# Optimization experiments

Hardware: AMD Instinct MI355X
Metric: run time of the kernel (lower is better)

Reference implementation:

```python
import jax, jax.numpy as jnp
import numpy as np
import math

B, L, D, P = 2, 2048, 256, 32
PI = math.pi


def _layernorm(x, g, b, eps=1e-5):
    m = x.mean(-1, keepdims=True)
    v = x.var(-1, keepdims=True)
    return (x - m) / jnp.sqrt(v + eps) * g + b


def setup_inputs() -> dict:
    key = jax.random.key(0)
    ks = jax.random.split(key, 16)
    sd = 1.0 / math.sqrt(D)
    f32 = jnp.float32
    inp = {
        "x": jax.random.normal(ks[0], (B, L, D), f32),
        # key_encoder: Linear(D, P)
        "key_W": jax.random.normal(ks[1], (D, P), f32) * sd,
        "key_b": jnp.zeros((P,), f32),
        # value_encoder: Linear(D, D)
        "val_W": jax.random.normal(ks[2], (D, D), f32) * sd,
        "val_b": jnp.zeros((D,), f32),
        # refiner: LayerNorm(D), Linear(D, 2D), GELU, Linear(2D, D)
        "ln1_g": jnp.ones((D,), f32),
        "ln1_b": jnp.zeros((D,), f32),
        "W1": jax.random.normal(ks[3], (D, 2 * D), f32) * sd,
        "b1": jnp.zeros((2 * D,), f32),
        "W2": jax.random.normal(ks[4], (2 * D, D), f32) * (1.0 / math.sqrt(2 * D)),
        "b2": jnp.zeros((D,), f32),
        # to_out: LayerNorm(D), Linear(D, D)
        "ln2_g": jnp.ones((D,), f32),
        "ln2_b": jnp.zeros((D,), f32),
        "Wo": jax.random.normal(ks[5], (D, D), f32) * sd,
        "bo": jnp.zeros((D,), f32),
    }
    return inp


def reference(x, key_W, key_b, val_W, val_b, ln1_g, ln1_b, W1, b1, W2, b2,
              ln2_g, ln2_b, Wo, bo):
    # key phases in (-pi, pi); phasor exp(i*theta) handled as (cos, sin)
    phases = jnp.tanh(x @ key_W + key_b) * PI          # (B, L, P)
    values = x @ val_W + val_b                          # (B, L, D)

    cos_p = jnp.cos(phases)
    sin_p = jnp.sin(phases)
    # torch.roll(shifts=1, dims=1) then zero the first position -> shift right, row 0 = 0
    zrow = jnp.zeros_like(cos_p[:, :1])
    cos_s = jnp.concatenate([zrow, cos_p[:, :-1]], axis=1)
    sin_s = jnp.concatenate([zrow, sin_p[:, :-1]], axis=1)

    # odd positions hold values
    vmask = (jnp.arange(L) % 2 == 1).astype(x.dtype)    # (L,)
    mv = values * vmask[None, :, None]                  # (B, L, D)

    # bind: outer product phasor (P) x value (D); real/imag parts
    bound_re = cos_s[..., None] * mv[:, :, None, :]     # (B, L, P, D)
    bound_im = sin_s[..., None] * mv[:, :, None, :]
    mem_re = jnp.cumsum(bound_re, axis=1)
    mem_im = jnp.cumsum(bound_im, axis=1)

    # retrieve: Re[ memory * exp(-i*theta) ] summed over phases
    retrieved = (jnp.einsum('blpd,blp->bld', mem_re, cos_p)
                 + jnp.einsum('blpd,blp->bld', mem_im, sin_p))

    valid = jnp.maximum(jnp.cumsum(vmask), 1.0)         # (L,)
    retrieved = retrieved / (jnp.sqrt(valid)[None, :, None] * math.sqrt(P))

    h = _layernorm(retrieved, ln1_g, ln1_b)
    h = jax.nn.gelu(h @ W1 + b1, approximate=False)
    refined = h @ W2 + b2
    out = x + (_layernorm(refined, ln2_g, ln2_b) @ Wo + bo)
    return out
```

## Files before the change

### kernel.cpp

```cpp
#include <hip/hip_runtime.h>
#include <math.h>

#define BB 2
#define LL 2048
#define DD 256
#define PP 32
#define NC 64
#define PI_F 3.14159265358979323846f

typedef __attribute__((ext_vector_type(8))) short bf16x8;
typedef __attribute__((ext_vector_type(4))) float f32x4;
typedef unsigned short ushort_t;
typedef unsigned int uint_t;

__device__ inline ushort_t f2bf(float x) {
    uint_t u = __float_as_uint(x);
    uint_t r = (u + 0x7fffu + ((u >> 16) & 1u)) >> 16;
    return (ushort_t)r;
}

__global__ __launch_bounds__(256) void prep_key_kernel(
    const float* __restrict__ W1, const float* __restrict__ W2,
    const float* __restrict__ Wo, const float* __restrict__ valW,
    const float* __restrict__ x, const float* __restrict__ key_W,
    const float* __restrict__ key_b,
    ushort_t* __restrict__ W1t, ushort_t* __restrict__ W2t,
    ushort_t* __restrict__ Wot, ushort_t* __restrict__ valWt,
    float2* __restrict__ ph)
{
    const int bid = blockIdx.x;
    const int t = threadIdx.x;
    if (bid < 96) {
        __shared__ float T[64][65];
        const float* W; ushort_t* Wt; int K, N, tile;
        if (bid < 32)      { W = W1;   Wt = W1t;   K = 256; N = 512; tile = bid; }
        else if (bid < 64) { W = W2;   Wt = W2t;   K = 512; N = 256; tile = bid - 32; }
        else if (bid < 80) { W = Wo;   Wt = Wot;   K = 256; N = 256; tile = bid - 64; }
        else               { W = valW; Wt = valWt; K = 256; N = 256; tile = bid - 80; }
        const int ntiles = N / 64;
        const int k0 = (tile / ntiles) * 64, n0 = (tile % ntiles) * 64;
        {
            const int rr = t >> 2, cb = (t & 3) * 16;
            #pragma unroll
            for (int i = 0; i < 16; i += 4) {
                const float4 v = *(const float4*)&W[(k0 + rr) * N + n0 + cb + i];
                T[rr][cb + i + 0] = v.x; T[rr][cb + i + 1] = v.y;
                T[rr][cb + i + 2] = v.z; T[rr][cb + i + 3] = v.w;
            }
        }
        __syncthreads();
        {
            const int n = t >> 2, kb = (t & 3) * 16;
            #pragma unroll
            for (int i = 0; i < 16; ++i)
                Wt[(n0 + n) * K + k0 + kb + i] = f2bf(T[kb + i][n]);
        }
    } else {
        __shared__ float xs[256][8];
        const int row0 = (bid - 96) * 8;
        #pragma unroll
        for (int i = 0; i < 8; ++i)
            xs[t][i] = x[(row0 + i) * DD + t];
        __syncthreads();
        const int r = t >> 5, p = t & 31;
        float a = key_b[p];
        #pragma unroll 8
        for (int k = 0; k < DD; ++k)
            a += xs[k][r] * key_W[k * PP + p];
        a = tanhf(a) * PI_F;
        float sn, cs;
        sincosf(a, &sn, &cs);
        ph[(row0 + r) * PP + p] = make_float2(cs, sn);
    }
}

__global__ __launch_bounds__(256) void valbind_kernel(
    const float* __restrict__ x, const float2* __restrict__ ph,
    const ushort_t* __restrict__ valWt, const float* __restrict__ val_b,
    float* __restrict__ values_odd, float* __restrict__ M)
{
    __shared__ ushort_t xsb[16][264];
    __shared__ ushort_t VdT[128][40];
    __shared__ ushort_t phsT[64][40];

    const int tid = threadIdx.x;
    const int bid = blockIdx.x;
    const int b  = bid >> 7;
    const int rem = bid & 127;
    const int c  = rem >> 1;
    const int dh = rem & 1;
    const int base = b * LL;
    const int r0 = 32 * c;

    {
        const int j = tid >> 4, cb = (tid & 15) * 16;
        const float* src = &x[(long)(base + r0 + 2 * j + 1) * DD + cb];
        ushort_t tmp[16];
        #pragma unroll
        for (int i = 0; i < 4; ++i) {
            const float4 v = *(const float4*)&src[i * 4];
            tmp[i*4+0] = f2bf(v.x); tmp[i*4+1] = f2bf(v.y);
            tmp[i*4+2] = f2bf(v.z); tmp[i*4+3] = f2bf(v.w);
        }
        *(uint4*)&xsb[j][cb]     = *(uint4*)&tmp[0];
        *(uint4*)&xsb[j][cb + 8] = *(uint4*)&tmp[8];
    }
    {
        const int j = tid >> 4, qb = (tid & 15) * 4;
        const float4 v = *(const float4*)((const float*)ph +
                              (long)(base + r0 + 2 * j) * 64 + qb);
        phsT[qb + 0][j] = f2bf(v.x);
        phsT[qb + 1][j] = f2bf(v.y);
        phsT[qb + 2][j] = f2bf(v.z);
        phsT[qb + 3][j] = f2bf(v.w);
    }
    for (int e = tid; e < 64 * 16; e += 256)
        phsT[e >> 4][16 + (e & 15)] = 0;
    for (int e = tid; e < 128 * 16; e += 256)
        VdT[e >> 4][16 + (e & 15)] = 0;
    __syncthreads();

    const int wv = tid >> 6, lane = tid & 63;
    const int qd = lane >> 4, mc = lane & 15;

    f32x4 va0 = {0.f,0.f,0.f,0.f}, va1 = {0.f,0.f,0.f,0.f};
    const int dloc0 = wv * 32 + mc, dloc1 = dloc0 + 16;
    const int n0g = dh * 128 + dloc0, n1g = n0g + 16;
    const ushort_t* B0 = &valWt[(long)n0g * 256];
    const ushort_t* B1 = &valWt[(long)n1g * 256];
    #pragma unroll
    for (int ks = 0; ks < 8; ++ks) {
        const bf16x8 a  = *(const bf16x8*)&xsb[mc][ks * 32 + qd * 8];
        const bf16x8 b0 = *(const bf16x8*)&B0[ks * 32 + qd * 8];
        const bf16x8 b1 = *(const bf16x8*)&B1[ks * 32 + qd * 8];
        va0 = __builtin_amdgcn_mfma_f32_16x16x32_bf16(a, b0, va0, 0, 0, 0);
        va1 = __builtin_amdgcn_mfma_f32_16x16x32_bf16(a, b1, va1, 0, 0, 0);
    }
    {
        const float bb0 = val_b[n0g], bb1 = val_b[n1g];
        #pragma unroll
        for (int r = 0; r < 4; ++r) {
            const int j = qd * 4 + r;
            const float v0 = va0[r] + bb0, v1 = va1[r] + bb1;
            const long rowo = ((long)(b * NC + c) * 16 + j) * DD;
            values_odd[rowo + n0g] = v0;
            values_odd[rowo + n1g] = v1;
            VdT[dloc0][j] = f2bf(v0);
            VdT[dloc1][j] = f2bf(v1);
        }
    }
    __syncthreads();

    const bf16x8 a2 = *(const bf16x8*)&phsT[wv * 16 + mc][qd * 8];
    f32x4 macc[8];
    #pragma unroll
    for (int nf = 0; nf < 8; ++nf) {
        f32x4 z = {0.f,0.f,0.f,0.f};
        const bf16x8 b2 = *(const bf16x8*)&VdT[nf * 16 + mc][qd * 8];
        macc[nf] = __builtin_amdgcn_mfma_f32_16x16x32_bf16(a2, b2, z, 0, 0, 0);
    }
    #pragma unroll
    for (int nf = 0; nf < 8; ++nf) {
        #pragma unroll
        for (int r = 0; r < 4; ++r) {
            const int q = wv * 16 + qd * 4 + r;
            M[((long)(b * NC + c) * 64 + q) * 256 + dh * 128 + nf * 16 + mc]
                = macc[nf][r];
        }
    }
}

__global__ __launch_bounds__(256) void prefix_kernel(float* __restrict__ M)
{
    const int tid = threadIdx.x;
    const int b   = blockIdx.x >> 6;
    const int col = (blockIdx.x & 63) * 256 + tid;
    float run = 0.f;
    #pragma unroll 4
    for (int c = 0; c < NC; ++c) {
        const long a = ((long)(b * NC + c)) * 16384 + col;
        const float tmp = M[a];
        M[a] = run;
        run += tmp;
    }
}

__device__ inline float red32(float v) {
    v += __shfl_xor(v, 16, 32);
    v += __shfl_xor(v, 8, 32);
    v += __shfl_xor(v, 4, 32);
    v += __shfl_xor(v, 2, 32);
    v += __shfl_xor(v, 1, 32);
    return v;
}

__global__ __launch_bounds__(256) void retrieve_kernel(
    const float2* __restrict__ ph, const float* __restrict__ values_odd,
    const float* __restrict__ Mpre,
    const float* __restrict__ ln1_g, const float* __restrict__ ln1_b,
    ushort_t* __restrict__ rhat)
{
    __shared__ float phT[64][10];
    __shared__ float S[16][10];
    __shared__ float ref[8][264];

    const int tid = threadIdx.x;
    const int b   = blockIdx.x >> 8;
    const int lt  = blockIdx.x & 255;
    const int l0  = lt * 8;
    const int base = b * LL;
    const int c     = l0 >> 5;
    const int l0loc = l0 & 31;
    const int jcnt  = l0loc / 2 + 4;

    const float* phf = (const float*)ph;
    #pragma unroll
    for (int k = 0; k < 2; ++k) {
        const int e = tid + k * 256;
        const int r = e >> 6, q = e & 63;
        phT[q][r] = phf[(base + l0 + r) * 64 + q];
    }
    __syncthreads();

    if (tid < 128) {
        const int l = tid & 7, j = tid >> 3;
        const float* ps = &phf[(base + 32 * c + 2 * j) * 64];
        float s = 0.f;
        #pragma unroll 8
        for (int q = 0; q < 64; ++q)
            s += phT[q][l] * ps[q];
        if (2 * j + 1 > l0loc + l) s = 0.f;
        S[j][l] = s;
    }

    const int g = tid >> 6;
    const int d4 = (tid & 63) * 4;
    float4 acc0 = make_float4(0.f,0.f,0.f,0.f);
    float4 acc1 = make_float4(0.f,0.f,0.f,0.f);
    {
        const float* Mc = &Mpre[((long)(b * NC + c)) * 16384 + d4];
        #pragma unroll 8
        for (int q = 0; q < 64; ++q) {
            const float4 m = *(const float4*)&Mc[q * DD];
            const float2 ss = *(const float2*)&phT[q][2 * g];
            acc0.x += m.x * ss.x; acc0.y += m.y * ss.x;
            acc0.z += m.z * ss.x; acc0.w += m.w * ss.x;
            acc1.x += m.x * ss.y; acc1.y += m.y * ss.y;
            acc1.z += m.z * ss.y; acc1.w += m.w * ss.y;
        }
    }
    __syncthreads();

    for (int j = 0; j < jcnt; ++j) {
        const float4 v = *(const float4*)
            &values_odd[((long)(b * NC + c) * 16 + j) * DD + d4];
        const float2 ss = *(const float2*)&S[j][2 * g];
        acc0.x += v.x * ss.x; acc0.y += v.y * ss.x;
        acc0.z += v.z * ss.x; acc0.w += v.w * ss.x;
        acc1.x += v.x * ss.y; acc1.y += v.y * ss.y;
        acc1.z += v.z * ss.y; acc1.w += v.w * ss.y;
    }

    {
        const float invP = 0.17677669529663687f;
        const int la = l0 + 2 * g;
        int va = (la + 1) / 2; if (va < 1) va = 1;
        const float sc0 = invP * rsqrtf((float)va);
        int vb = (la + 2) / 2; if (vb < 1) vb = 1;
        const float sc1 = invP * rsqrtf((float)vb);
        *(float4*)&ref[2 * g][d4] = make_float4(acc0.x*sc0, acc0.y*sc0, acc0.z*sc0, acc0.w*sc0);
        *(float4*)&ref[2 * g + 1][d4] = make_float4(acc1.x*sc1, acc1.y*sc1, acc1.z*sc1, acc1.w*sc1);
    }
    __syncthreads();

    {
        const long row0 = (long)blockIdx.x * 8;
        const int r = tid >> 5, lane = tid & 31;
        float v[8], s = 0.f, sq = 0.f;
        #pragma unroll
        for (int i = 0; i < 8; ++i) {
            v[i] = ref[r][lane + 32 * i];
            s += v[i]; sq += v[i] * v[i];
        }
        s = red32(s); sq = red32(sq);
        const float m = s * (1.f / 256.f);
        const float inv = rsqrtf(sq * (1.f / 256.f) - m * m + 1e-5f);
        #pragma unroll
        for (int i = 0; i < 8; ++i) {
            const int cc = lane + 32 * i;
            rhat[(row0 + r) * DD + cc] = f2bf((v[i] - m) * inv * ln1_g[cc] + ln1_b[cc]);
        }
    }
}

template<int K, int N, int MODE>
__global__ __launch_bounds__(256) void mfma_gemm(
    const ushort_t* __restrict__ A, const ushort_t* __restrict__ Bt,
    const float* __restrict__ bias, const float* __restrict__ resid,
    void* __restrict__ out)
{
    __shared__ ushort_t As[16][136];
    __shared__ ushort_t Bs[64][136];
    const int tid = threadIdx.x;
    const int mt = blockIdx.x & 255;
    const int nt = blockIdx.x >> 8;
    const int m0 = mt * 16, n0 = nt * 64;
    const int wv = tid >> 6, lane = tid & 63;
    const int qd = lane >> 4, mc = lane & 15;

    f32x4 acc = {0.f, 0.f, 0.f, 0.f};

    const int ar = tid >> 4, ak = (tid & 15) * 8;
    const int bn = tid >> 2, bk = (tid & 3) * 32;

    for (int k0 = 0; k0 < K; k0 += 128) {
        __syncthreads();
        *(uint4*)&As[ar][ak] = *(const uint4*)&A[(long)(m0 + ar) * K + k0 + ak];
        {
            const ushort_t* src = &Bt[(long)(n0 + bn) * K + k0 + bk];
            *(uint4*)&Bs[bn][bk +  0] = *(const uint4*)&src[0];
            *(uint4*)&Bs[bn][bk +  8] = *(const uint4*)&src[8];
            *(uint4*)&Bs[bn][bk + 16] = *(const uint4*)&src[16];
            *(uint4*)&Bs[bn][bk + 24] = *(const uint4*)&src[24];
        }
        __syncthreads();
        #pragma unroll
        for (int ko = 0; ko < 128; ko += 32) {
            const bf16x8 a = *(const bf16x8*)&As[mc][ko + qd * 8];
            const bf16x8 b = *(const bf16x8*)&Bs[wv * 16 + mc][ko + qd * 8];
            acc = __builtin_amdgcn_mfma_f32_16x16x32_bf16(a, b, acc, 0, 0, 0);
        }
    }

    const int nn = n0 + wv * 16 + mc;
    const float bb = bias[nn];
    #pragma unroll
    for (int r = 0; r < 4; ++r) {
        const long row = m0 + qd * 4 + r;
        float v = acc[r] + bb;
        if (MODE == 0) {
            v = 0.5f * v * (1.f + erff(v * 0.70710678118654752f));
            ((ushort_t*)out)[row * N + nn] = f2bf(v);
        } else {
            ((float*)out)[row * N + nn] = v + resid[row * N + nn];
        }
    }
}

__global__ __launch_bounds__(256) void gemm2ln_kernel(
    const ushort_t* __restrict__ h, const ushort_t* __restrict__ W2t,
    const float* __restrict__ b2, const float* __restrict__ ln2_g,
    const float* __restrict__ ln2_b, ushort_t* __restrict__ shat)
{
    __shared__ ushort_t As[16][72];
    __shared__ ushort_t Bs[256][72];
    __shared__ float Ct[16][264];

    const int tid = threadIdx.x;
    const int m0 = blockIdx.x * 16;
    const int wv = tid >> 6, lane = tid & 63;
    const int qd = lane >> 4, mc = lane & 15;

    f32x4 acc[4];
    #pragma unroll
    for (int nf = 0; nf < 4; ++nf) acc[nf] = (f32x4){0.f,0.f,0.f,0.f};

    const int sr = tid >> 3, sk = (tid & 7) * 8;

    for (int k0 = 0; k0 < 512; k0 += 64) {
        __syncthreads();
        if (tid < 128)
            *(uint4*)&As[sr][sk] = *(const uint4*)&h[(long)(m0 + sr) * 512 + k0 + sk];
        #pragma unroll
        for (int rr = 0; rr < 8; ++rr) {
            const int n = rr * 32 + (tid >> 3);
            *(uint4*)&Bs[n][sk] = *(const uint4*)&W2t[(long)n * 512 + k0 + sk];
        }
        __syncthreads();
        #pragma unroll
        for (int ks = 0; ks < 2; ++ks) {
            const bf16x8 a = *(const bf16x8*)&As[mc][ks * 32 + qd * 8];
            #pragma unroll
            for (int nf = 0; nf < 4; ++nf) {
                const bf16x8 b = *(const bf16x8*)&Bs[wv * 64 + nf * 16 + mc][ks * 32 + qd * 8];
                acc[nf] = __builtin_amdgcn_mfma_f32_16x16x32_bf16(a, b, acc[nf], 0, 0, 0);
            }
        }
    }

    #pragma unroll
    for (int nf = 0; nf < 4; ++nf) {
        const int n = wv * 64 + nf * 16 + mc;
        const float bb = b2[n];
        #pragma unroll
        for (int r = 0; r < 4; ++r)
            Ct[qd * 4 + r][n] = acc[nf][r] + bb;
    }
    __syncthreads();

    {
        const int row = tid >> 4, cg = (tid & 15) * 16;
        float s = 0.f, sq = 0.f;
        #pragma unroll
        for (int i = 0; i < 16; ++i) {
            const float v = Ct[row][cg + i];
            s += v; sq += v * v;
        }
        s  += __shfl_xor(s, 1, 16);  sq += __shfl_xor(sq, 1, 16);
        s  += __shfl_xor(s, 2, 16);  sq += __shfl_xor(sq, 2, 16);
        s  += __shfl_xor(s, 4, 16);  sq += __shfl_xor(sq, 4, 16);
        s  += __shfl_xor(s, 8, 16);  sq += __shfl_xor(sq, 8, 16);
        const float m = s * (1.f / 256.f);
        const float inv = rsqrtf(sq * (1.f / 256.f) - m * m + 1e-5f);
        #pragma unroll
        for (int i = 0; i < 16; ++i) {
            const int cc = cg + i;
            shat[(long)(m0 + row) * DD + cc] =
                f2bf((Ct[row][cc] - m) * inv * ln2_g[cc] + ln2_b[cc]);
        }
    }
}

extern "C" void kernel_launch(void* const* d_in, const int* in_sizes, int n_in,
                              void* d_out, int out_size, void* d_ws, size_t ws_size,
                              hipStream_t stream)
{
    const float* x     = (const float*)d_in[0];
    const float* key_W = (const float*)d_in[1];
    const float* key_b = (const float*)d_in[2];
    const float* val_W = (const float*)d_in[3];
    const float* val_b = (const float*)d_in[4];
    const float* ln1_g = (const float*)d_in[5];
    const float* ln1_b = (const float*)d_in[6];
    const float* W1    = (const float*)d_in[7];
    const float* b1    = (const float*)d_in[8];
    const float* W2    = (const float*)d_in[9];
    const float* b2    = (const float*)d_in[10];
    const float* ln2_g = (const float*)d_in[11];
    const float* ln2_b = (const float*)d_in[12];
    const float* Wo    = (const float*)d_in[13];
    const float* bo    = (const float*)d_in[14];
    float* outp = (float*)d_out;

    float* ws = (float*)d_ws;
    float2* ph         = (float2*)ws;
    float*  values_odd = ws + 262144;
    float*  M          = values_odd + 524288;
    ushort_t* rhat_b   = (ushort_t*)(M + 2097152);
    ushort_t* W1t      = (ushort_t*)(M + 2097152 + 524288);
    ushort_t* W2t      = W1t + 131072;
    ushort_t* Wot      = W2t + 131072;
    ushort_t* valWt    = Wot + 65536;
    ushort_t* h_b      = (ushort_t*)M;
    ushort_t* shat_b   = (ushort_t*)(M + 1048576);

    prep_key_kernel<<<608, 256, 0, stream>>>(W1, W2, Wo, val_W, x, key_W, key_b,
                                             W1t, W2t, Wot, valWt, ph);
    valbind_kernel<<<256, 256, 0, stream>>>(x, ph, valWt, val_b, values_odd, M);
    prefix_kernel<<<BB * 64, 256, 0, stream>>>(M);
    retrieve_kernel<<<BB * (LL / 8), 256, 0, stream>>>(ph, values_odd, M,
                                                       ln1_g, ln1_b, rhat_b);
    mfma_gemm<256, 512, 0><<<256 * 8, 256, 0, stream>>>(rhat_b, W1t, b1, nullptr, h_b);
    gemm2ln_kernel<<<256, 256, 0, stream>>>(h_b, W2t, b2, ln2_g, ln2_b, shat_b);
    mfma_gemm<256, 256, 2><<<256 * 4, 256, 0, stream>>>(shat_b, Wot, bo, x, outp);
}
```

Baseline: 141.7 us.

## Move retrieve stage onto bf16 MFMA with transposed memory layout and parallel prefix

The retrieve kernel now does its work with bf16 MFMA instead of scalar FMA loops. It handles 16 rows per block and reads a transposed chunk memory (Mt) and transposed bf16 odd values that valbind writes through shared memory. The prefix scan is split into four segments per column to raise parallelism, and prep_key stages key_W in shared memory. The aim is to cut retrieve's FMA and memory cost and the serial scan latency, at the cost of bf16 rounding on the memory and phase products.

Result: faster. 133.1 us (-6.1%).

```diff
diff --git a/kernel.cpp b/kernel.cpp
--- a/kernel.cpp
+++ b/kernel.cpp
@@ -57,16 +57,25 @@
         }
     } else {
         __shared__ float xs[256][8];
+        __shared__ float kw[256][33];
         const int row0 = (bid - 96) * 8;
         #pragma unroll
         for (int i = 0; i < 8; ++i)
             xs[t][i] = x[(row0 + i) * DD + t];
+        #pragma unroll
+        for (int p4 = 0; p4 < 8; ++p4) {
+            const int idx4 = p4 * 256 + t;
+            const int k = idx4 >> 3, pc = (idx4 & 7) * 4;
+            const float4 v = *(const float4*)&key_W[k * 32 + pc];
+            kw[k][pc + 0] = v.x; kw[k][pc + 1] = v.y;
+            kw[k][pc + 2] = v.z; kw[k][pc + 3] = v.w;
+        }
         __syncthreads();
         const int r = t >> 5, p = t & 31;
         float a = key_b[p];
         #pragma unroll 8
         for (int k = 0; k < DD; ++k)
-            a += xs[k][r] * key_W[k * PP + p];
+            a += xs[k][r] * kw[k][p];
         a = tanhf(a) * PI_F;
         float sn, cs;
         sincosf(a, &sn, &cs);
@@ -77,11 +86,12 @@
 __global__ __launch_bounds__(256) void valbind_kernel(
     const float* __restrict__ x, const float2* __restrict__ ph,
     const ushort_t* __restrict__ valWt, const float* __restrict__ val_b,
-    float* __restrict__ values_odd, float* __restrict__ M)
+    ushort_t* __restrict__ VoddT, float* __restrict__ Mt)
 {
     __shared__ ushort_t xsb[16][264];
     __shared__ ushort_t VdT[128][40];
     __shared__ ushort_t phsT[64][40];
+    __shared__ float    Ms[128][68];
 
     const int tid = threadIdx.x;
     const int bid = blockIdx.x;
@@ -141,12 +151,8 @@
         #pragma unroll
         for (int r = 0; r < 4; ++r) {
             const int j = qd * 4 + r;
-            const float v0 = va0[r] + bb0, v1 = va1[r] + bb1;
-            const long rowo = ((long)(b * NC + c) * 16 + j) * DD;
-            values_odd[rowo + n0g] = v0;
-            values_odd[rowo + n1g] = v1;
-            VdT[dloc0][j] = f2bf(v0);
-            VdT[dloc1][j] = f2bf(v1);
+            VdT[dloc0][j] = f2bf(va0[r] + bb0);
+            VdT[dloc1][j] = f2bf(va1[r] + bb1);
         }
     }
     __syncthreads();
@@ -164,132 +170,189 @@
         #pragma unroll
         for (int r = 0; r < 4; ++r) {
             const int q = wv * 16 + qd * 4 + r;
-            M[((long)(b * NC + c) * 64 + q) * 256 + dh * 128 + nf * 16 + mc]
-                = macc[nf][r];
-        }
+            Ms[nf * 16 + mc][q] = macc[nf][r];
+        }
+    }
+    __syncthreads();
+
+    {
+        float* dst = &Mt[((long)(b * NC + c) * 256 + dh * 128) * 64];
+        #pragma unroll
+        for (int p = 0; p < 8; ++p) {
+            const int idx4 = p * 256 + tid;
+            const int dloc = idx4 >> 4, q4 = (idx4 & 15) * 4;
+            const float4 v = *(const float4*)&Ms[dloc][q4];
+            *(float4*)&dst[dloc * 64 + q4] = v;
+        }
+    }
+    if (tid < 128) {
+        ushort_t* vd = &VoddT[((long)(b * NC + c) * 256 + dh * 128 + tid) * 16];
+        *(uint4*)&vd[0] = *(const uint4*)&VdT[tid][0];
+        *(uint4*)&vd[8] = *(const uint4*)&VdT[tid][8];
     }
 }
 
 __global__ __launch_bounds__(256) void prefix_kernel(float* __restrict__ M)
 {
+    __shared__ float segsum[4][64];
     const int tid = threadIdx.x;
-    const int b   = blockIdx.x >> 6;
-    const int col = (blockIdx.x & 63) * 256 + tid;
+    const int b  = blockIdx.x >> 8;
+    const int cg = blockIdx.x & 255;
+    const int col = cg * 64 + (tid & 63);
+    const int seg = tid >> 6;
+    const long base = (long)b * NC * 16384 + col;
+
+    float v[16], s = 0.f;
+    #pragma unroll
+    for (int i = 0; i < 16; ++i) {
+        v[i] = M[base + (long)(seg * 16 + i) * 16384];
+        s += v[i];
+    }
+    segsum[seg][tid & 63] = s;
+    __syncthreads();
     float run = 0.f;
-    #pragma unroll 4
-    for (int c = 0; c < NC; ++c) {
-        const long a = ((long)(b * NC + c)) * 16384 + col;
-        const float tmp = M[a];
+    #pragma unroll
+    for (int sg = 0; sg < 3; ++sg)
+        if (sg < seg) run += segsum[sg][tid & 63];
+    #pragma unroll
+    for (int i = 0; i < 16; ++i) {
+        const long a = base + (long)(seg * 16 + i) * 16384;
         M[a] = run;
-        run += tmp;
-    }
-}
-
-__device__ inline float red32(float v) {
-    v += __shfl_xor(v, 16, 32);
-    v += __shfl_xor(v, 8, 32);
-    v += __shfl_xor(v, 4, 32);
-    v += __shfl_xor(v, 2, 32);
-    v += __shfl_xor(v, 1, 32);
-    return v;
+        run += v[i];
+    }
 }
 
 __global__ __launch_bounds__(256) void retrieve_kernel(
-    const float2* __restrict__ ph, const float* __restrict__ values_odd,
-    const float* __restrict__ Mpre,
+    const float* __restrict__ ph, const float* __restrict__ Mpre,
+    const ushort_t* __restrict__ VoddT,
     const float* __restrict__ ln1_g, const float* __restrict__ ln1_b,
     ushort_t* __restrict__ rhat)
 {
-    __shared__ float phT[64][10];
-    __shared__ float S[16][10];
-    __shared__ float ref[8][264];
+    __shared__ ushort_t Bs_m[256][72];
+    __shared__ ushort_t Bs_v[256][32];
+    __shared__ ushort_t As_ph[16][72];
+    __shared__ ushort_t Bs_sh[16][72];
+    __shared__ ushort_t As_p[16][32];
+    __shared__ float    ref[16][264];
 
     const int tid = threadIdx.x;
-    const int b   = blockIdx.x >> 8;
-    const int lt  = blockIdx.x & 255;
-    const int l0  = lt * 8;
-    const int base = b * LL;
-    const int c     = l0 >> 5;
-    const int l0loc = l0 & 31;
-    const int jcnt  = l0loc / 2 + 4;
-
-    const float* phf = (const float*)ph;
-    #pragma unroll
-    for (int k = 0; k < 2; ++k) {
-        const int e = tid + k * 256;
-        const int r = e >> 6, q = e & 63;
-        phT[q][r] = phf[(base + l0 + r) * 64 + q];
-    }
-    __syncthreads();
-
-    if (tid < 128) {
-        const int l = tid & 7, j = tid >> 3;
-        const float* ps = &phf[(base + 32 * c + 2 * j) * 64];
-        float s = 0.f;
-        #pragma unroll 8
-        for (int q = 0; q < 64; ++q)
-            s += phT[q][l] * ps[q];
-        if (2 * j + 1 > l0loc + l) s = 0.f;
-        S[j][l] = s;
-    }
-
-    const int g = tid >> 6;
-    const int d4 = (tid & 63) * 4;
-    float4 acc0 = make_float4(0.f,0.f,0.f,0.f);
-    float4 acc1 = make_float4(0.f,0.f,0.f,0.f);
-    {
-        const float* Mc = &Mpre[((long)(b * NC + c)) * 16384 + d4];
-        #pragma unroll 8
-        for (int q = 0; q < 64; ++q) {
-            const float4 m = *(const float4*)&Mc[q * DD];
-            const float2 ss = *(const float2*)&phT[q][2 * g];
-            acc0.x += m.x * ss.x; acc0.y += m.y * ss.x;
-            acc0.z += m.z * ss.x; acc0.w += m.w * ss.x;
-            acc1.x += m.x * ss.y; acc1.y += m.y * ss.y;
-            acc1.z += m.z * ss.y; acc1.w += m.w * ss.y;
-        }
-    }
-    __syncthreads();
-
-    for (int j = 0; j < jcnt; ++j) {
-        const float4 v = *(const float4*)
-            &values_odd[((long)(b * NC + c) * 16 + j) * DD + d4];
-        const float2 ss = *(const float2*)&S[j][2 * g];
-        acc0.x += v.x * ss.x; acc0.y += v.y * ss.x;
-        acc0.z += v.z * ss.x; acc0.w += v.w * ss.x;
-        acc1.x += v.x * ss.y; acc1.y += v.y * ss.y;
-        acc1.z += v.z * ss.y; acc1.w += v.w * ss.y;
-    }
-
-    {
-        const float invP = 0.17677669529663687f;
-        const int la = l0 + 2 * g;
-        int va = (la + 1) / 2; if (va < 1) va = 1;
-        const float sc0 = invP * rsqrtf((float)va);
-        int vb = (la + 2) / 2; if (vb < 1) vb = 1;
-        const float sc1 = invP * rsqrtf((float)vb);
-        *(float4*)&ref[2 * g][d4] = make_float4(acc0.x*sc0, acc0.y*sc0, acc0.z*sc0, acc0.w*sc0);
-        *(float4*)&ref[2 * g + 1][d4] = make_float4(acc1.x*sc1, acc1.y*sc1, acc1.z*sc1, acc1.w*sc1);
-    }
-    __syncthreads();
-
-    {
-        const long row0 = (long)blockIdx.x * 8;
-        const int r = tid >> 5, lane = tid & 31;
-        float v[8], s = 0.f, sq = 0.f;
-        #pragma unroll
-        for (int i = 0; i < 8; ++i) {
-            v[i] = ref[r][lane + 32 * i];
-            s += v[i]; sq += v[i] * v[i];
-        }
-        s = red32(s); sq = red32(sq);
+    const int b = blockIdx.x >> 7;
+    const int c = (blockIdx.x >> 1) & 63;
+    const int h = blockIdx.x & 1;
+    const int l0g = 32 * c + 16 * h;
+    const long rowbase = (long)b * LL + l0g;
+
+    {
+        const float* src = &Mpre[(long)(b * NC + c) * 16384];
+        #pragma unroll
+        for (int p = 0; p < 16; ++p) {
+            const int idx4 = p * 256 + tid;
+            const int d = idx4 >> 4, q4 = (idx4 & 15) * 4;
+            const float4 v = *(const float4*)&src[idx4 * 4];
+            ushort_t tmp[4] = {f2bf(v.x), f2bf(v.y), f2bf(v.z), f2bf(v.w)};
+            *(uint2*)&Bs_m[d][q4] = *(uint2*)tmp;
+        }
+    }
+    {
+        const int r = tid >> 4, q4 = (tid & 15) * 4;
+        const float4 v = *(const float4*)&ph[(rowbase + r) * 64 + q4];
+        ushort_t t0[4] = {f2bf(v.x), f2bf(v.y), f2bf(v.z), f2bf(v.w)};
+        *(uint2*)&As_ph[r][q4] = *(uint2*)t0;
+        const float4 w = *(const float4*)&ph[((long)b * LL + 32 * c + 2 * r) * 64 + q4];
+        ushort_t t1[4] = {f2bf(w.x), f2bf(w.y), f2bf(w.z), f2bf(w.w)};
+        *(uint2*)&Bs_sh[r][q4] = *(uint2*)t1;
+    }
+    {
+        const ushort_t* src = &VoddT[(long)(b * NC + c) * 4096];
+        const int j0 = (tid & 1) * 8;
+        *(uint4*)&Bs_v[tid >> 1][j0] = *(const uint4*)&src[tid * 8];
+        *(uint4*)&Bs_v[(tid + 256) >> 1][j0] = *(const uint4*)&src[(tid + 256) * 8];
+        *(uint4*)&Bs_v[tid][16] = make_uint4(0, 0, 0, 0);
+        *(uint4*)&Bs_v[tid][24] = make_uint4(0, 0, 0, 0);
+        As_p[tid >> 4][16 + (tid & 15)] = 0;
+    }
+    __syncthreads();
+
+    const int wv = tid >> 6, lane = tid & 63;
+    const int qd = lane >> 4, mc = lane & 15;
+
+    {
+        f32x4 sacc = {0.f, 0.f, 0.f, 0.f};
+        #pragma unroll
+        for (int ks = 0; ks < 2; ++ks) {
+            const bf16x8 a  = *(const bf16x8*)&As_ph[mc][ks * 32 + qd * 8];
+            const bf16x8 bb = *(const bf16x8*)&Bs_sh[mc][ks * 32 + qd * 8];
+            sacc = __builtin_amdgcn_mfma_f32_16x16x32_bf16(a, bb, sacc, 0, 0, 0);
+        }
+        if (wv == 0) {
+            #pragma unroll
+            for (int r = 0; r < 4; ++r) {
+                const int l = qd * 4 + r;
+                As_p[l][mc] = (2 * mc + 1 <= 16 * h + l) ? f2bf(sacc[r])
+                                                         : (ushort_t)0;
+            }
+        }
+    }
+
+    f32x4 acc[4];
+    #pragma unroll
+    for (int i = 0; i < 4; ++i) acc[i] = (f32x4){0.f, 0.f, 0.f, 0.f};
+    #pragma unroll
+    for (int i = 0; i < 4; ++i) {
+        const int d0 = wv * 64 + i * 16;
+        #pragma unroll
+        for (int ks = 0; ks < 2; ++ks) {
+            const bf16x8 a  = *(const bf16x8*)&As_ph[mc][ks * 32 + qd * 8];
+            const bf16x8 bb = *(const bf16x8*)&Bs_m[d0 + mc][ks * 32 + qd * 8];
+            acc[i] = __builtin_amdgcn_mfma_f32_16x16x32_bf16(a, bb, acc[i], 0, 0, 0);
+        }
+    }
+    __syncthreads();
+
+    {
+        const bf16x8 a2 = *(const bf16x8*)&As_p[mc][qd * 8];
+        #pragma unroll
+        for (int i = 0; i < 4; ++i) {
+            const int d0 = wv * 64 + i * 16;
+            const bf16x8 b2 = *(const bf16x8*)&Bs_v[d0 + mc][qd * 8];
+            acc[i] = __builtin_amdgcn_mfma_f32_16x16x32_bf16(a2, b2, acc[i], 0, 0, 0);
+        }
+    }
+
+    #pragma unroll
+    for (int r = 0; r < 4; ++r) {
+        const int l = qd * 4 + r;
+        int va = (l0g + l + 1) >> 1; if (va < 1) va = 1;
+        const float sc = 0.17677669529663687f * rsqrtf((float)va);
+        #pragma unroll
+        for (int i = 0; i < 4; ++i)
+            ref[l][wv * 64 + i * 16 + mc] = acc[i][r] * sc;
+    }
+    __syncthreads();
+
+    {
+        const int row = tid >> 4, cg = (tid & 15) * 16;
+        float s = 0.f, sq = 0.f;
+        #pragma unroll
+        for (int i = 0; i < 16; ++i) {
+            const float v = ref[row][cg + i];
+            s += v; sq += v * v;
+        }
+        s += __shfl_xor(s, 1, 16);  sq += __shfl_xor(sq, 1, 16);
+        s += __shfl_xor(s, 2, 16);  sq += __shfl_xor(sq, 2, 16);
+        s += __shfl_xor(s, 4, 16);  sq += __shfl_xor(sq, 4, 16);
+        s += __shfl_xor(s, 8, 16);  sq += __shfl_xor(sq, 8, 16);
         const float m = s * (1.f / 256.f);
         const float inv = rsqrtf(sq * (1.f / 256.f) - m * m + 1e-5f);
-        #pragma unroll
-        for (int i = 0; i < 8; ++i) {
-            const int cc = lane + 32 * i;
-            rhat[(row0 + r) * DD + cc] = f2bf((v[i] - m) * inv * ln1_g[cc] + ln1_b[cc]);
-        }
+        ushort_t o16[16];
+        #pragma unroll
+        for (int i = 0; i < 16; ++i) {
+            const int cc = cg + i;
+            o16[i] = f2bf((ref[row][cc] - m) * inv * ln1_g[cc] + ln1_b[cc]);
+        }
+        ushort_t* dst = &rhat[(rowbase + row) * DD + cg];
+        *(uint4*)&dst[0] = *(uint4*)&o16[0];
+        *(uint4*)&dst[8] = *(uint4*)&o16[8];
     }
 }
 
@@ -443,23 +506,23 @@
     float* outp = (float*)d_out;
 
     float* ws = (float*)d_ws;
-    float2* ph         = (float2*)ws;
-    float*  values_odd = ws + 262144;
-    float*  M          = values_odd + 524288;
-    ushort_t* rhat_b   = (ushort_t*)(M + 2097152);
-    ushort_t* W1t      = (ushort_t*)(M + 2097152 + 524288);
-    ushort_t* W2t      = W1t + 131072;
-    ushort_t* Wot      = W2t + 131072;
-    ushort_t* valWt    = Wot + 65536;
-    ushort_t* h_b      = (ushort_t*)M;
-    ushort_t* shat_b   = (ushort_t*)(M + 1048576);
+    float*  ph      = ws;
+    float*  Mt      = ws + 262144;
+    ushort_t* VoddT = (ushort_t*)(Mt + 2097152);
+    ushort_t* rhat_b = VoddT + 524288;
+    ushort_t* W1t   = rhat_b + 1048576;
+    ushort_t* W2t   = W1t + 131072;
+    ushort_t* Wot   = W2t + 131072;
+    ushort_t* valWt = Wot + 65536;
+    ushort_t* h_b    = (ushort_t*)Mt;
+    ushort_t* shat_b = (ushort_t*)(Mt + 1048576);
 
     prep_key_kernel<<<608, 256, 0, stream>>>(W1, W2, Wo, val_W, x, key_W, key_b,
-                                             W1t, W2t, Wot, valWt, ph);
-    valbind_kernel<<<256, 256, 0, stream>>>(x, ph, valWt, val_b, values_odd, M);
-    prefix_kernel<<<BB * 64, 256, 0, stream>>>(M);
-    retrieve_kernel<<<BB * (LL / 8), 256, 0, stream>>>(ph, values_odd, M,
-                                                       ln1_g, ln1_b, rhat_b);
+                                             W1t, W2t, Wot, valWt, (float2*)ph);
+    valbind_kernel<<<256, 256, 0, stream>>>(x, (const float2*)ph, valWt, val_b,
+                                            VoddT, Mt);
+    prefix_kernel<<<512, 256, 0, stream>>>(Mt);
+    retrieve_kernel<<<256, 256, 0, stream>>>(ph, Mt, VoddT, ln1_g, ln1_b, rhat_b);
     mfma_gemm<256, 512, 0><<<256 * 8, 256, 0, stream>>>(rhat_b, W1t, b1, nullptr, h_b);
     gemm2ln_kernel<<<256, 256, 0, stream>>>(h_b, W2t, b2, ln2_g, ln2_b, shat_b);
     mfma_gemm<256, 256, 2><<<256 * 4, 256, 0, stream>>>(shat_b, Wot, bo, x, outp);
```
